# Kernel optimization log

Measured on AMD Instinct MI355X. Metric: run time of the kernel, lower is better.

The kernel has to match this reference:

```python
import jax, jax.numpy as jnp
import numpy as np

N, L, D_IN = 8192, 32, 256   # total paths, max path len, token+method embed
E, H, T, C = 128, 128, 128, 2  # encode_size, hidden_dim, test_vector_size, label_count
G = 1024                      # number of methods (groups)
LN_EPS = 1e-5


def _lstm_last_hidden(xs, lengths, Wih, Whh, bih, bhh):
    """Single-layer LSTM over padded [N,L,E]; returns h at t=length-1 per row (packed-sequence h_n)."""
    xs_t = jnp.transpose(xs, (1, 0, 2))  # [L, N, E]
    n = xs.shape[0]
    h0 = jnp.zeros((n, H), xs.dtype)
    c0 = jnp.zeros((n, H), xs.dtype)

    def step(carry, inp):
        h, c = carry
        x_t, t = inp
        gates = x_t @ Wih.T + bih + h @ Whh.T + bhh  # [N, 4H], torch gate order i,f,g,o
        i, f, g, o = jnp.split(gates, 4, axis=-1)
        c_new = jax.nn.sigmoid(f) * c + jax.nn.sigmoid(i) * jnp.tanh(g)
        h_new = jax.nn.sigmoid(o) * jnp.tanh(c_new)
        valid = (t < lengths)[:, None]  # freeze state past each path's length
        return (jnp.where(valid, h_new, h), jnp.where(valid, c_new, c)), None

    (h_last, _), _ = jax.lax.scan(step, (h0, c0), (xs_t, jnp.arange(L)))
    return h_last  # [N, H]


def setup_inputs() -> dict:
    key = jax.random.key(0)
    ks = jax.random.split(key, 10)
    rng = np.random.default_rng(0)

    inputs = jax.random.normal(ks[0], (N, L, D_IN), dtype=jnp.float32)
    path_lengths = jnp.asarray(rng.integers(1, L + 1, size=N), dtype=jnp.int32)
    # sorted segment ids, every group non-empty (torch.split groups are contiguous and >=1)
    ids = np.sort(np.concatenate([np.arange(G), rng.integers(0, G, size=N - G)]))
    segment_ids = jnp.asarray(ids, dtype=jnp.int32)

    s = 0.05
    W_in = jax.random.normal(ks[1], (E, D_IN), dtype=jnp.float32) * s
    ln_gamma = jnp.ones((E,), jnp.float32)
    ln_beta = jnp.zeros((E,), jnp.float32)
    Wih = jax.random.normal(ks[2], (4 * H, E), dtype=jnp.float32) * s
    Whh = jax.random.normal(ks[3], (4 * H, H), dtype=jnp.float32) * s
    bih = jax.random.normal(ks[4], (4 * H,), dtype=jnp.float32) * s
    bhh = jax.random.normal(ks[5], (4 * H,), dtype=jnp.float32) * s
    attn_param = jax.random.normal(ks[6], (H,), dtype=jnp.float32) * s
    W_out = jax.random.normal(ks[7], (T, H), dtype=jnp.float32) * s
    W_cls = jax.random.normal(ks[8], (C, T), dtype=jnp.float32) * s

    return {"inputs": inputs, "path_lengths": path_lengths, "segment_ids": segment_ids,
            "W_in": W_in, "ln_gamma": ln_gamma, "ln_beta": ln_beta,
            "Wih": Wih, "Whh": Whh, "bih": bih, "bhh": bhh,
            "attn_param": attn_param, "W_out": W_out, "W_cls": W_cls}


def reference(inputs, path_lengths, segment_ids, W_in, ln_gamma, ln_beta,
              Wih, Whh, bih, bhh, attn_param, W_out, W_cls):
    # input projection + layernorm + tanh (dropout disabled, p=0)
    x = inputs @ W_in.T  # [N, L, E]
    mu = jnp.mean(x, axis=-1, keepdims=True)
    var = jnp.mean((x - mu) ** 2, axis=-1, keepdims=True)
    x = jnp.tanh((x - mu) * jax.lax.rsqrt(var + LN_EPS) * ln_gamma + ln_beta)

    h = _lstm_last_hidden(x, path_lengths, Wih, Whh, bih, bhh)  # [N, H]

    # segmented softmax attention + mean over each group's paths
    logits = h @ attn_param  # [N]
    m = jax.ops.segment_max(logits, segment_ids, num_segments=G)
    e = jnp.exp(logits - m[segment_ids])
    Z = jax.ops.segment_sum(e, segment_ids, num_segments=G)
    attn = e / Z[segment_ids]  # per-group softmax weights
    wsum = jax.ops.segment_sum(attn[:, None] * h, segment_ids, num_segments=G)  # [G, H]
    counts = jax.ops.segment_sum(jnp.ones_like(logits), segment_ids, num_segments=G)
    code = wsum / counts[:, None]  # torch.mean divides by group size

    code_vectors = code @ W_out.T  # [G, T]
    outputs = code_vectors @ W_cls.T  # [G, C]
    return outputs, code_vectors, attn_param
```

## Files before the change

### kernel.cpp

```cpp
#include <hip/hip_runtime.h>


#define NPATH 8192
#define LMAX  32
#define DIN   256
#define EDIM  128
#define HDIM  128
#define NGRP  1024
#define NTOK  (NPATH * LMAX)
#define NCHUNK 512

typedef __attribute__((ext_vector_type(8))) short short8;
typedef __attribute__((ext_vector_type(4))) short s16x4;
typedef __attribute__((ext_vector_type(4))) float f32x4;

__device__ __forceinline__ unsigned short f2bf(float f) {
    unsigned int x = __float_as_uint(f);
    x += 0x7fffu + ((x >> 16) & 1u);
    return (unsigned short)(x >> 16);
}
__device__ __forceinline__ float sigmoid_f(float x) {
    return __fdividef(1.f, 1.f + __expf(-x));
}
__device__ __forceinline__ float tanh_f(float x) {
    float ax = fabsf(x);
    float t = __expf(-2.f * ax);
    float r = __fdividef(1.f - t, 1.f + t);
    return copysignf(r, x);
}

__global__ __launch_bounds__(512) void k0_sort(const int* __restrict__ lens,
                                               int* __restrict__ perm) {
    __shared__ int hist[LMAX];
    __shared__ int offs[LMAX];
    const int tid = threadIdx.x;
    if (tid < LMAX) hist[tid] = 0;
    __syncthreads();
    for (int i = tid; i < NPATH; i += 512) atomicAdd(&hist[lens[i] - 1], 1);
    __syncthreads();
    if (tid == 0) {
        int s = 0;
        for (int b = 0; b < LMAX; ++b) { offs[b] = s; s += hist[b]; }
    }
    __syncthreads();
    for (int i = tid; i < NPATH; i += 512) {
        int p = atomicAdd(&offs[lens[i] - 1], 1);
        perm[p] = i;
    }
}

#define K1_ROWS 128
#define K1_PAD  264
__global__ __launch_bounds__(512) void k1_proj(
    const float* __restrict__ inp, const float* __restrict__ Win,
    const float* __restrict__ gam, const float* __restrict__ bet,
    unsigned short* __restrict__ xt)
{
    __shared__ short As[K1_ROWS * K1_PAD];
    __shared__ short Bs[EDIM * K1_PAD];
    const int tid = threadIdx.x;
    const long m0 = (long)blockIdx.x * K1_ROWS;

    #pragma unroll
    for (int i = 0; i < 16; ++i) {
        int chunk = i * 512 + tid;
        int row = chunk >> 6, c4 = chunk & 63;
        float4 v = *(const float4*)&Win[row * DIN + c4 * 4];
        s16x4 s = { (short)f2bf(v.x), (short)f2bf(v.y), (short)f2bf(v.z), (short)f2bf(v.w) };
        *(s16x4*)&Bs[row * K1_PAD + c4 * 4] = s;
    }
    #pragma unroll
    for (int i = 0; i < 16; ++i) {
        int chunk = i * 512 + tid;
        int row = chunk >> 6, c4 = chunk & 63;
        float4 v = *(const float4*)&inp[(m0 + row) * DIN + c4 * 4];
        s16x4 s = { (short)f2bf(v.x), (short)f2bf(v.y), (short)f2bf(v.z), (short)f2bf(v.w) };
        *(s16x4*)&As[row * K1_PAD + c4 * 4] = s;
    }
    __syncthreads();

    const int w = tid >> 6, lane = tid & 63, q = lane >> 4, c = lane & 15;
    const f32x4 fzero = {0.f, 0.f, 0.f, 0.f};
    f32x4 acc[8];
    #pragma unroll
    for (int nt = 0; nt < 8; ++nt) acc[nt] = fzero;

    const short* arow = &As[(w * 16 + c) * K1_PAD + q * 8];
    const short* brow = &Bs[c * K1_PAD + q * 8];
    #pragma unroll
    for (int ks = 0; ks < 8; ++ks) {
        short8 a = *(const short8*)(arow + ks * 32);
        #pragma unroll
        for (int nt = 0; nt < 8; ++nt) {
            short8 b = *(const short8*)(brow + nt * 16 * K1_PAD + ks * 32);
            acc[nt] = __builtin_amdgcn_mfma_f32_16x16x32_bf16(a, b, acc[nt], 0, 0, 0);
        }
    }

    float gr[8], br[8];
    #pragma unroll
    for (int nt = 0; nt < 8; ++nt) { int col = nt * 16 + c; gr[nt] = gam[col]; br[nt] = bet[col]; }
    #pragma unroll
    for (int r = 0; r < 4; ++r) {
        float s = 0.f, ss = 0.f;
        #pragma unroll
        for (int nt = 0; nt < 8; ++nt) { float v = acc[nt][r]; s += v; ss += v * v; }
        #pragma unroll
        for (int m = 1; m < 16; m <<= 1) { s += __shfl_xor(s, m, 64); ss += __shfl_xor(ss, m, 64); }
        float mu = s * (1.f / 128.f);
        float var = ss * (1.f / 128.f) - mu * mu;
        float rstd = rsqrtf(var + 1e-5f);
        unsigned short* orow = &xt[(m0 + w * 16 + q * 4 + r) * EDIM];
        #pragma unroll
        for (int nt = 0; nt < 8; ++nt) {
            float v = (acc[nt][r] - mu) * rstd * gr[nt] + br[nt];
            orow[nt * 16 + c] = f2bf(tanh_f(v));
        }
    }
}

__global__ __launch_bounds__(512, 2) void k2_lstm(
    const unsigned short* __restrict__ xt,
    const float* __restrict__ Wih, const float* __restrict__ Whh,
    const float* __restrict__ bih, const float* __restrict__ bhh,
    const int* __restrict__ lens, const int* __restrict__ perm,
    float* __restrict__ h_last)
{
    __shared__ unsigned short wih_s[512 * 128];
    __shared__ unsigned short hb[2][16 * 128];
    __shared__ int pemb[16];
    __shared__ int lenb[16];
    const int tid = threadIdx.x;
    const int w = tid >> 6, lane = tid & 63, q = lane >> 4, c = lane & 15;
    const int xr = (c & 7) << 3;

    #pragma unroll
    for (int i = 0; i < 32; ++i) {
        int chunk = i * 512 + tid;
        int j = chunk >> 5, c4 = chunk & 31;
        float4 v = *(const float4*)&Wih[j * EDIM + c4 * 4];
        s16x4 s = { (short)f2bf(v.x), (short)f2bf(v.y), (short)f2bf(v.z), (short)f2bf(v.w) };
        *(s16x4*)&wih_s[j * 128 + ((c4 * 4) ^ ((j & 7) << 3))] = s;
    }

    short8 whf[4][4];
    float bs[4];
    #pragma unroll
    for (int g = 0; g < 4; ++g) {
        const int j = g * 128 + w * 16 + c;
        bs[g] = bih[j] + bhh[j];
        const float* ph = Whh + (long)j * HDIM + q * 8;
        #pragma unroll
        for (int ks = 0; ks < 4; ++ks) {
            float4 b0 = *(const float4*)(ph + ks * 32);
            float4 b1 = *(const float4*)(ph + ks * 32 + 4);
            short8 u;
            u[0] = (short)f2bf(b0.x); u[1] = (short)f2bf(b0.y);
            u[2] = (short)f2bf(b0.z); u[3] = (short)f2bf(b0.w);
            u[4] = (short)f2bf(b1.x); u[5] = (short)f2bf(b1.y);
            u[6] = (short)f2bf(b1.z); u[7] = (short)f2bf(b1.w);
            whf[g][ks] = u;
        }
    }

    int koff[4];
    #pragma unroll
    for (int ks = 0; ks < 4; ++ks) koff[ks] = (q * 8 + ks * 32) ^ xr;
    const unsigned short* wbase[4];
    #pragma unroll
    for (int g = 0; g < 4; ++g) wbase[g] = &wih_s[(g * 128 + w * 16 + c) * 128];

    for (int half = 0; half < 2; ++half) {
        const int cid = half ? (NCHUNK - 1 - (int)blockIdx.x) : (int)blockIdx.x;
        const int r0 = cid * 16;
        if (tid < 16) { int p = perm[r0 + tid]; pemb[tid] = p; lenb[tid] = lens[p]; }
        { s16x4 z = {0, 0, 0, 0}; *(s16x4*)&hb[0][tid * 4] = z; }
        __syncthreads();

        int steps = 1;
        #pragma unroll
        for (int i = 0; i < 16; ++i) steps = (lenb[i] > steps) ? lenb[i] : steps;
        int lenr[4];
        #pragma unroll
        for (int r = 0; r < 4; ++r) lenr[r] = lenb[q * 4 + r];
        const unsigned short* xrow = xt + (long)pemb[c] * (LMAX * EDIM) + q * 8;

        float c_reg[4] = {0.f, 0.f, 0.f, 0.f};
        float h_reg[4] = {0.f, 0.f, 0.f, 0.f};
        short8 xf[4];
        #pragma unroll
        for (int ks = 0; ks < 4; ++ks) xf[ks] = *(const short8*)(xrow + ks * 32);

        int cur = 0;
        for (int t = 0; t < steps; ++t) {
            f32x4 acc[4];
            #pragma unroll
            for (int g = 0; g < 4; ++g) {
                f32x4 a = {bs[g], bs[g], bs[g], bs[g]};
                acc[g] = a;
            }
            if (t) {
                short8 ha[4];
                #pragma unroll
                for (int ks = 0; ks < 4; ++ks)
                    ha[ks] = *(const short8*)&hb[cur][c * 128 + koff[ks]];
                #pragma unroll
                for (int ks = 0; ks < 4; ++ks)
                    #pragma unroll
                    for (int g = 0; g < 4; ++g)
                        acc[g] = __builtin_amdgcn_mfma_f32_16x16x32_bf16(ha[ks], whf[g][ks], acc[g], 0, 0, 0);
            }
            #pragma unroll
            for (int ks = 0; ks < 4; ++ks)
                #pragma unroll
                for (int g = 0; g < 4; ++g) {
                    short8 b = *(const short8*)(wbase[g] + koff[ks]);
                    acc[g] = __builtin_amdgcn_mfma_f32_16x16x32_bf16(xf[ks], b, acc[g], 0, 0, 0);
                }
            {
                const int tn = (t + 1 < steps) ? (t + 1) : t;
                const unsigned short* xp = xrow + (long)tn * EDIM;
                #pragma unroll
                for (int ks = 0; ks < 4; ++ks) xf[ks] = *(const short8*)(xp + ks * 32);
            }
            const int nxt = cur ^ 1;
            #pragma unroll
            for (int r = 0; r < 4; ++r) {
                float cn = sigmoid_f(acc[1][r]) * c_reg[r]
                         + sigmoid_f(acc[0][r]) * tanh_f(acc[2][r]);
                float hn = sigmoid_f(acc[3][r]) * tanh_f(cn);
                if (t < lenr[r]) { c_reg[r] = cn; h_reg[r] = hn; }
                const int row = q * 4 + r;
                hb[nxt][row * 128 + ((w * 16 + c) ^ ((row & 7) << 3))] = f2bf(h_reg[r]);
            }
            __syncthreads();
            cur = nxt;
        }
        #pragma unroll
        for (int r = 0; r < 4; ++r)
            h_last[(long)pemb[q * 4 + r] * HDIM + w * 16 + c] = h_reg[r];
        if (half == 0) __syncthreads();
    }
}

__global__ __launch_bounds__(64) void k3_attn(
    const float* __restrict__ h_last, const int* __restrict__ seg,
    const float* __restrict__ attn, const float* __restrict__ Wout,
    const float* __restrict__ Wcls, float* __restrict__ out)
{
    __shared__ float code_s[128];
    const int g = blockIdx.x, l = threadIdx.x;

    int lo, hi;
    { int a = 0, b = NPATH; while (a < b) { int m = (a + b) >> 1; if (seg[m] < g) a = m + 1; else b = m; } lo = a; }
    { int a = lo, b = NPATH; while (a < b) { int m = (a + b) >> 1; if (seg[m] < g + 1) a = m + 1; else b = m; } hi = a; }

    float a0 = attn[l], a1 = attn[l + 64];
    float mrun = -1e30f, Z = 0.f;
    for (int n = lo; n < hi; ++n) {
        const float* hr = &h_last[(long)n * HDIM];
        float v = hr[l] * a0 + hr[l + 64] * a1;
        #pragma unroll
        for (int m = 1; m < 64; m <<= 1) v += __shfl_xor(v, m, 64);
        float nm = fmaxf(mrun, v);
        Z = Z * __expf(mrun - nm) + __expf(v - nm);
        mrun = nm;
    }
    float w0 = 0.f, w1 = 0.f;
    for (int n = lo; n < hi; ++n) {
        const float* hr = &h_last[(long)n * HDIM];
        float v = hr[l] * a0 + hr[l + 64] * a1;
        #pragma unroll
        for (int m = 1; m < 64; m <<= 1) v += __shfl_xor(v, m, 64);
        float at = __expf(v - mrun) / Z;
        w0 += at * hr[l]; w1 += at * hr[l + 64];
    }
    float inv_cnt = (hi > lo) ? 1.f / (float)(hi - lo) : 0.f;
    code_s[l] = w0 * inv_cnt; code_s[l + 64] = w1 * inv_cnt;
    __syncthreads();

    float cv0 = 0.f, cv1 = 0.f;
    for (int k = 0; k < 128; ++k) {
        float ck = code_s[k];
        cv0 += ck * Wout[l * 128 + k];
        cv1 += ck * Wout[(l + 64) * 128 + k];
    }
    out[2048 + g * 128 + l]      = cv0;
    out[2048 + g * 128 + l + 64] = cv1;

    float p0 = cv0 * Wcls[l] + cv1 * Wcls[l + 64];
    float p1 = cv0 * Wcls[128 + l] + cv1 * Wcls[128 + l + 64];
    #pragma unroll
    for (int m = 1; m < 64; m <<= 1) { p0 += __shfl_xor(p0, m, 64); p1 += __shfl_xor(p1, m, 64); }
    if (l == 0) { out[g * 2 + 0] = p0; out[g * 2 + 1] = p1; }
    if (g == 0) { out[133120 + l] = attn[l]; out[133120 + 64 + l] = attn[l + 64]; }
}

extern "C" void kernel_launch(void* const* d_in, const int* in_sizes, int n_in,
                              void* d_out, int out_size, void* d_ws, size_t ws_size,
                              hipStream_t stream) {
    const float* inp  = (const float*)d_in[0];
    const int*   lens = (const int*)d_in[1];
    const int*   seg  = (const int*)d_in[2];
    const float* Win  = (const float*)d_in[3];
    const float* gam  = (const float*)d_in[4];
    const float* bet  = (const float*)d_in[5];
    const float* Wih  = (const float*)d_in[6];
    const float* Whh  = (const float*)d_in[7];
    const float* bih  = (const float*)d_in[8];
    const float* bhh  = (const float*)d_in[9];
    const float* attn = (const float*)d_in[10];
    const float* Wout = (const float*)d_in[11];
    const float* Wcls = (const float*)d_in[12];

    unsigned short* xt = (unsigned short*)d_ws;
    float* h_last = (float*)((char*)d_ws + (size_t)NTOK * EDIM * 2);
    int* perm = (int*)((char*)d_ws + (size_t)NTOK * EDIM * 2
                                   + (size_t)NPATH * HDIM * 4);

    hipLaunchKernelGGL(k0_sort, dim3(1), dim3(512), 0, stream, lens, perm);
    hipLaunchKernelGGL(k1_proj, dim3(NTOK / K1_ROWS), dim3(512), 0, stream, inp, Win, gam, bet, xt);
    hipLaunchKernelGGL(k2_lstm, dim3(NCHUNK / 2), dim3(512), 0, stream,
                       xt, Wih, Whh, bih, bhh, lens, perm, h_last);
    hipLaunchKernelGGL(k3_attn, dim3(NGRP), dim3(64), 0, stream, h_last, seg, attn, Wout, Wcls,
                       (float*)d_out);
}
```

Baseline: 529.9 us.

## Store projected tokens time-major in sorted order and stage LSTM inputs via LDS

The sort kernel now also emits an inverse permutation, and the projection kernel writes each token into a time-major slab indexed by sorted path slot. Each LSTM chunk of 16 paths then reads one contiguous 4KB block per step, prefetched by all threads into a double-buffered LDS tile instead of per-lane strided global loads. This aims at better coalescing and at hiding latency in the recurrent loop, at the cost of extra LDS and a scattered write pattern in the projection kernel. The tanh approximation is also simplified, trading the abs/copysign form for one with possible overflow behaviour at large negative inputs.

```diff
diff --git a/kernel.cpp b/kernel.cpp
--- a/kernel.cpp
+++ b/kernel.cpp
@@ -9,6 +9,7 @@
 #define NGRP  1024
 #define NTOK  (NPATH * LMAX)
 #define NCHUNK 512
+#define XSLAB ((long)NPATH * EDIM)
 
 typedef __attribute__((ext_vector_type(8))) short short8;
 typedef __attribute__((ext_vector_type(4))) short s16x4;
@@ -23,29 +24,46 @@
     return __fdividef(1.f, 1.f + __expf(-x));
 }
 __device__ __forceinline__ float tanh_f(float x) {
-    float ax = fabsf(x);
-    float t = __expf(-2.f * ax);
-    float r = __fdividef(1.f - t, 1.f + t);
-    return copysignf(r, x);
+    float t = __expf(-2.f * x);
+    return __fdividef(2.f, 1.f + t) - 1.f;
 }
 
 __global__ __launch_bounds__(512) void k0_sort(const int* __restrict__ lens,
-                                               int* __restrict__ perm) {
-    __shared__ int hist[LMAX];
-    __shared__ int offs[LMAX];
+                                               int* __restrict__ perm,
+                                               int* __restrict__ inv) {
+    __shared__ int hw[8][LMAX];
+    __shared__ int startg[8][LMAX];
+    __shared__ int colsum[LMAX];
+    __shared__ int binoff[LMAX];
     const int tid = threadIdx.x;
-    if (tid < LMAX) hist[tid] = 0;
-    __syncthreads();
-    for (int i = tid; i < NPATH; i += 512) atomicAdd(&hist[lens[i] - 1], 1);
+    const int w = tid >> 6, lane = tid & 63;
+    if (lane < LMAX) hw[w][lane] = 0;
+    __syncthreads();
+    for (int i = tid; i < NPATH; i += 512)
+        atomicAdd(&hw[w][lens[i] - 1], 1);
+    __syncthreads();
+    if (tid < LMAX) {
+        int s = 0;
+        #pragma unroll
+        for (int ww = 0; ww < 8; ++ww) { startg[ww][tid] = s; s += hw[ww][tid]; }
+        colsum[tid] = s;
+    }
     __syncthreads();
     if (tid == 0) {
         int s = 0;
-        for (int b = 0; b < LMAX; ++b) { offs[b] = s; s += hist[b]; }
+        for (int b = 0; b < LMAX; ++b) { binoff[b] = s; s += colsum[b]; }
+    }
+    __syncthreads();
+    if (tid < LMAX) {
+        #pragma unroll
+        for (int ww = 0; ww < 8; ++ww) startg[ww][tid] += binoff[tid];
     }
     __syncthreads();
     for (int i = tid; i < NPATH; i += 512) {
-        int p = atomicAdd(&offs[lens[i] - 1], 1);
+        int b = lens[i] - 1;
+        int p = atomicAdd(&startg[w][b], 1);
         perm[p] = i;
+        inv[i] = p;
     }
 }
 
@@ -54,7 +72,7 @@
 __global__ __launch_bounds__(512) void k1_proj(
     const float* __restrict__ inp, const float* __restrict__ Win,
     const float* __restrict__ gam, const float* __restrict__ bet,
-    unsigned short* __restrict__ xt)
+    const int* __restrict__ inv, unsigned short* __restrict__ xt)
 {
     __shared__ short As[K1_ROWS * K1_PAD];
     __shared__ short Bs[EDIM * K1_PAD];
@@ -100,6 +118,9 @@
     float gr[8], br[8];
     #pragma unroll
     for (int nt = 0; nt < 8; ++nt) { int col = nt * 16 + c; gr[nt] = gam[col]; br[nt] = bet[col]; }
+    const int tok0 = w * 16 + q * 4;
+    const int slot = inv[(int)((m0 + tok0) >> 5)];
+    const int tbase = tok0 & 31;
     #pragma unroll
     for (int r = 0; r < 4; ++r) {
         float s = 0.f, ss = 0.f;
@@ -110,7 +131,7 @@
         float mu = s * (1.f / 128.f);
         float var = ss * (1.f / 128.f) - mu * mu;
         float rstd = rsqrtf(var + 1e-5f);
-        unsigned short* orow = &xt[(m0 + w * 16 + q * 4 + r) * EDIM];
+        unsigned short* orow = &xt[(long)(tbase + r) * XSLAB + (long)slot * EDIM];
         #pragma unroll
         for (int nt = 0; nt < 8; ++nt) {
             float v = (acc[nt][r] - mu) * rstd * gr[nt] + br[nt];
@@ -128,6 +149,7 @@
 {
     __shared__ unsigned short wih_s[512 * 128];
     __shared__ unsigned short hb[2][16 * 128];
+    __shared__ unsigned short xb[2][16 * 128];
     __shared__ int pemb[16];
     __shared__ int lenb[16];
     const int tid = threadIdx.x;
@@ -170,11 +192,19 @@
     #pragma unroll
     for (int g = 0; g < 4; ++g) wbase[g] = &wih_s[(g * 128 + w * 16 + c) * 128];
 
+    const int srow = tid >> 5;
+    const int scol = (tid * 4) & 127;
+    const int sdst = srow * 128 + (scol ^ ((srow & 7) << 3));
+
     for (int half = 0; half < 2; ++half) {
         const int cid = half ? (NCHUNK - 1 - (int)blockIdx.x) : (int)blockIdx.x;
         const int r0 = cid * 16;
         if (tid < 16) { int p = perm[r0 + tid]; pemb[tid] = p; lenb[tid] = lens[p]; }
         { s16x4 z = {0, 0, 0, 0}; *(s16x4*)&hb[0][tid * 4] = z; }
+        {
+            s16x4 v = *(const s16x4*)&xt[(long)r0 * EDIM + tid * 4];
+            *(s16x4*)&xb[0][sdst] = v;
+        }
         __syncthreads();
 
         int steps = 1;
@@ -183,16 +213,15 @@
         int lenr[4];
         #pragma unroll
         for (int r = 0; r < 4; ++r) lenr[r] = lenb[q * 4 + r];
-        const unsigned short* xrow = xt + (long)pemb[c] * (LMAX * EDIM) + q * 8;
 
         float c_reg[4] = {0.f, 0.f, 0.f, 0.f};
         float h_reg[4] = {0.f, 0.f, 0.f, 0.f};
-        short8 xf[4];
-        #pragma unroll
-        for (int ks = 0; ks < 4; ++ks) xf[ks] = *(const short8*)(xrow + ks * 32);
 
         int cur = 0;
         for (int t = 0; t < steps; ++t) {
+            const int tn = (t + 1 < steps) ? (t + 1) : t;
+            s16x4 xg = *(const s16x4*)&xt[(long)tn * XSLAB + (long)r0 * EDIM + tid * 4];
+
             f32x4 acc[4];
             #pragma unroll
             for (int g = 0; g < 4; ++g) {
@@ -211,19 +240,17 @@
                         acc[g] = __builtin_amdgcn_mfma_f32_16x16x32_bf16(ha[ks], whf[g][ks], acc[g], 0, 0, 0);
             }
             #pragma unroll
-            for (int ks = 0; ks < 4; ++ks)
+            for (int ks = 0; ks < 4; ++ks) {
+                short8 xa = *(const short8*)&xb[cur][c * 128 + koff[ks]];
                 #pragma unroll
                 for (int g = 0; g < 4; ++g) {
                     short8 b = *(const short8*)(wbase[g] + koff[ks]);
-                    acc[g] = __builtin_amdgcn_mfma_f32_16x16x32_bf16(xf[ks], b, acc[g], 0, 0, 0);
+                    acc[g] = __builtin_amdgcn_mfma_f32_16x16x32_bf16(xa, b, acc[g], 0, 0, 0);
                 }
-            {
-                const int tn = (t + 1 < steps) ? (t + 1) : t;
-                const unsigned short* xp = xrow + (long)tn * EDIM;
-                #pragma unroll
-                for (int ks = 0; ks < 4; ++ks) xf[ks] = *(const short8*)(xp + ks * 32);
             }
             const int nxt = cur ^ 1;
+            *(s16x4*)&xb[nxt][sdst] = xg;
+
             #pragma unroll
             for (int r = 0; r < 4; ++r) {
                 float cn = sigmoid_f(acc[1][r]) * c_reg[r]
@@ -317,9 +344,10 @@
     float* h_last = (float*)((char*)d_ws + (size_t)NTOK * EDIM * 2);
     int* perm = (int*)((char*)d_ws + (size_t)NTOK * EDIM * 2
                                    + (size_t)NPATH * HDIM * 4);
-
-    hipLaunchKernelGGL(k0_sort, dim3(1), dim3(512), 0, stream, lens, perm);
-    hipLaunchKernelGGL(k1_proj, dim3(NTOK / K1_ROWS), dim3(512), 0, stream, inp, Win, gam, bet, xt);
+    int* inv  = perm + NPATH;
+
+    hipLaunchKernelGGL(k0_sort, dim3(1), dim3(512), 0, stream, lens, perm, inv);
+    hipLaunchKernelGGL(k1_proj, dim3(NTOK / K1_ROWS), dim3(512), 0, stream, inp, Win, gam, bet, inv, xt);
     hipLaunchKernelGGL(k2_lstm, dim3(NCHUNK / 2), dim3(512), 0, stream,
                        xt, Wih, Whh, bih, bhh, lens, perm, h_last);
     hipLaunchKernelGGL(k3_attn, dim3(NGRP), dim3(64), 0, stream, h_last, seg, attn, Wout, Wcls,
```

Measured after the change: 537.2 us. Within noise of the previous version (+1.4%).
